# Kernel optimization log

Hardware: AMD Instinct MI355X
Metric: run time of the kernel (lower is better)

The kernel has to match this reference:

```python
import jax, jax.numpy as jnp
import numpy as np

EPS_RHO = 1e-8
EPS_DEN = 1e-9


def _rho_signed_sqrt(x):
    return jnp.sqrt(jax.nn.relu(x) + EPS_RHO) - jnp.sqrt(jax.nn.relu(-x) + EPS_RHO)


def setup_inputs() -> dict:
    key = jax.random.key(0)
    ks = jax.random.split(key, 8)
    B, N, C, A = 2, 512, 1024, 64  # batch, seq, hidden_dim, attn_dim
    s_c = 1.0 / np.sqrt(C)
    s_a = 1.0 / np.sqrt(A)
    return {
        "X": jax.random.normal(ks[0], (B, N, C), jnp.float32),
        "Wq": jax.random.normal(ks[1], (A, C), jnp.float32) * s_c,   # Linear(C->A), no bias
        "Wk": jax.random.normal(ks[2], (A, C), jnp.float32) * s_c,   # Linear(C->A), no bias
        "Wphi": jax.random.normal(ks[3], (A,), jnp.float32) * s_a,   # Linear(A->1), no bias
        "Wy_w": jax.random.normal(ks[4], (C, C), jnp.float32) * s_c, # Linear(C->C)
        "Wy_b": jax.random.normal(ks[5], (C,), jnp.float32) * s_c,
        "We_w": jax.random.normal(ks[6], (C, A), jnp.float32) * s_a, # Linear(A->C)
        "We_b": jax.random.normal(ks[7], (C,), jnp.float32) * s_a,
    }


def reference(X, Wq, Wk, Wphi, Wy_w, Wy_b, We_w, We_b):
    # q, k: (B,N,A); Vy: (B,N,C)
    q = jnp.einsum('bnc,ac->bna', X, Wq)
    k = jnp.einsum('bnc,ac->bna', X, Wk)
    Vy = jnp.einsum('bnc,dc->bnd', X, Wy_w) + Wy_b

    # pairwise features e_ij = relu(rho(q_i + k_j)): (B,N,N,A)
    e = jax.nn.relu(_rho_signed_sqrt(q[:, :, None, :] + k[:, None, :, :]))

    # scores: (B,N,N); stable exp with per-row max (== online-softmax result)
    scores = jnp.einsum('bija,a->bij', e, Wphi)
    m = jnp.max(scores, axis=-1, keepdims=True)
    ex = jnp.exp(scores - m)
    denom = jnp.sum(ex, axis=-1)  # (B,N)

    # part1 = exp_scores @ Vy
    part1 = jnp.einsum('bij,bjc->bic', ex, Vy)
    # part2 = sum_j ex_ij * (We e_ij + be) = We(sum_j ex_ij e_ij) + be * denom  (We is linear)
    Ew = jnp.einsum('bij,bija->bia', ex, e)  # (B,N,A)
    part2 = jnp.einsum('bia,ca->bic', Ew, We_w) + We_b * denom[..., None]

    return (part1 + part2) / (denom[..., None] + EPS_DEN)
```

## Files before the change

kernel.cpp:

```cpp
#include <hip/hip_runtime.h>
#include <math.h>

#define EPS_RHO 1e-8f
#define EPS_DEN 1e-9f

constexpr int Bb = 2;
constexpr int Nn = 512;
constexpr int Cc = 1024;
constexpr int Aa = 64;
constexpr int TOK = Bb * Nn;
constexpr int KG  = 640;

typedef __attribute__((ext_vector_type(8))) short short8;
typedef __attribute__((ext_vector_type(4))) float f32x4;

__device__ __forceinline__ float e_fn(float s) {
    const float SQE = 9.9999994e-05f;
    return sqrtf(fmaxf(s, 0.f) + EPS_RHO) - SQE;
}

__device__ __forceinline__ short f2bf(float x) {
    union { float f; unsigned u; } v; v.f = x;
    unsigned r = v.u + 0x7FFFu + ((v.u >> 16) & 1u);
    return (short)(r >> 16);
}

__device__ __forceinline__ unsigned cvt_pk_bf16(float e0, float e1) {
    unsigned d;
    asm("v_cvt_pk_bf16_f32 %0, %1, %2" : "=v"(d) : "v"(e0), "v"(e1));
    return d;
}

__global__ __launch_bounds__(256) void mega_gemm(
    const float* __restrict__ X,
    const float* __restrict__ Wy_w,
    const float* __restrict__ Wq,
    const float* __restrict__ Wk,
    const float* __restrict__ Wy_b,
    short* __restrict__ Gt,
    float* __restrict__ qg,
    float* __restrict__ kTg)
{
    constexpr int K = 1024, BK = 64;
    __shared__ short As[64][72];
    __shared__ short Bs[64][72];

    int tid = threadIdx.x;
    int bm = blockIdx.y * 64;
    int bn = blockIdx.x * 64;
    int row = tid >> 2;
    int kq  = (tid & 3) << 4;

    const float* ag = X + (size_t)(bm + row) * K + kq;
    int nrow = bn + row;
    const float* bg;
    if (nrow < 1024)      bg = Wy_w + (size_t)nrow * K + kq;
    else if (nrow < 1088) bg = Wq + (size_t)(nrow - 1024) * K + kq;
    else                  bg = Wk + (size_t)(nrow - 1088) * K + kq;

    float4 ar[4], br[4];
    #pragma unroll
    for (int u = 0; u < 4; ++u) {
        ar[u] = *(const float4*)(ag + u * 4);
        br[u] = *(const float4*)(bg + u * 4);
    }

    int wid = tid >> 6, lane = tid & 63;
    int wm = (wid & 1) * 32, wn = (wid >> 1) * 32;
    int fr = lane & 15, fk = (lane >> 4) * 8;

    f32x4 acc[2][2] = {};

    for (int step = 0; step < K / BK; ++step) {
        __syncthreads();
        short tmpA[16], tmpB[16];
        #pragma unroll
        for (int u = 0; u < 4; ++u) {
            tmpA[u*4+0] = f2bf(ar[u].x); tmpA[u*4+1] = f2bf(ar[u].y);
            tmpA[u*4+2] = f2bf(ar[u].z); tmpA[u*4+3] = f2bf(ar[u].w);
            tmpB[u*4+0] = f2bf(br[u].x); tmpB[u*4+1] = f2bf(br[u].y);
            tmpB[u*4+2] = f2bf(br[u].z); tmpB[u*4+3] = f2bf(br[u].w);
        }
        *(short8*)&As[row][kq]     = *(short8*)&tmpA[0];
        *(short8*)&As[row][kq + 8] = *(short8*)&tmpA[8];
        *(short8*)&Bs[row][kq]     = *(short8*)&tmpB[0];
        *(short8*)&Bs[row][kq + 8] = *(short8*)&tmpB[8];
        __syncthreads();

        if (step + 1 < K / BK) {
            const float* ag2 = ag + (size_t)(step + 1) * BK;
            const float* bg2 = bg + (size_t)(step + 1) * BK;
            #pragma unroll
            for (int u = 0; u < 4; ++u) {
                ar[u] = *(const float4*)(ag2 + u * 4);
                br[u] = *(const float4*)(bg2 + u * 4);
            }
        }

        #pragma unroll
        for (int kk = 0; kk < 2; ++kk) {
            short8 af[2], bfr[2];
            #pragma unroll
            for (int mi = 0; mi < 2; ++mi)
                af[mi] = *(const short8*)&As[wm + mi * 16 + fr][kk * 32 + fk];
            #pragma unroll
            for (int ni = 0; ni < 2; ++ni)
                bfr[ni] = *(const short8*)&Bs[wn + ni * 16 + fr][kk * 32 + fk];
            #pragma unroll
            for (int mi = 0; mi < 2; ++mi)
                #pragma unroll
                for (int ni = 0; ni < 2; ++ni)
                    acc[mi][ni] = __builtin_amdgcn_mfma_f32_16x16x32_bf16(
                        af[mi], bfr[ni], acc[mi][ni], 0, 0, 0);
        }
    }

    int cr = (lane >> 4) * 4;
    int cc = lane & 15;
    if (bn < 1024) {
        #pragma unroll
        for (int mi = 0; mi < 2; ++mi)
            #pragma unroll
            for (int ni = 0; ni < 2; ++ni) {
                int c = bn + wn + ni * 16 + cc;
                float bv = Wy_b[c];
                #pragma unroll
                for (int r_ = 0; r_ < 4; ++r_) {
                    int t = bm + wm + mi * 16 + cr + r_;
                    int b = t >> 9, j = t & 511;
                    Gt[((size_t)(b * 1024 + c)) * KG + j] = f2bf(acc[mi][ni][r_] + bv);
                }
            }
    } else if (bn == 1024) {
        #pragma unroll
        for (int mi = 0; mi < 2; ++mi)
            #pragma unroll
            for (int ni = 0; ni < 2; ++ni) {
                int a = wn + ni * 16 + cc;
                #pragma unroll
                for (int r_ = 0; r_ < 4; ++r_) {
                    int t = bm + wm + mi * 16 + cr + r_;
                    qg[(size_t)t * Aa + a] = acc[mi][ni][r_];
                }
            }
    } else {
        #pragma unroll
        for (int mi = 0; mi < 2; ++mi)
            #pragma unroll
            for (int ni = 0; ni < 2; ++ni) {
                int a = wn + ni * 16 + cc;
                #pragma unroll
                for (int r_ = 0; r_ < 4; ++r_) {
                    int t = bm + wm + mi * 16 + cr + r_;
                    int b = t >> 9, j = t & 511;
                    kTg[((size_t)(b * 64 + a)) * 512 + j] = acc[mi][ni][r_];
                }
            }
    }
}

__global__ __launch_bounds__(256) void weprep(
    const float* __restrict__ We_w, short* __restrict__ Gt)
{
    int i = blockIdx.x * 256 + threadIdx.x;
    int s = i & 127;
    int c = (i >> 7) & 1023;
    int b = i >> 17;
    short v = (s < 64) ? f2bf(We_w[(size_t)c * Aa + s]) : (short)0;
    Gt[((size_t)(b * 1024 + c)) * KG + 512 + s] = v;
}

__global__ __launch_bounds__(256) void attn1_fused(
    const float* __restrict__ qg,
    const float* __restrict__ kTg,
    const float* __restrict__ Wphi,
    short* __restrict__ P,
    float* __restrict__ denomg)
{
    __shared__ __align__(16) float qs[Aa];
    __shared__ __align__(16) float wph[Aa];
    __shared__ __align__(16) short E[256][72];
    __shared__ __align__(16) float exs[256];
    __shared__ __align__(16) float red[256];
    __shared__ __align__(16) float ewp[4][Aa];

    int t = blockIdx.x;
    int b = t >> 9;
    int tid = threadIdx.x;

    if (tid < Aa) {
        qs[tid] = qg[(size_t)t * Aa + tid];
        wph[tid] = Wphi[tid];
    }
    __syncthreads();

    const float* kT = kTg + (size_t)b * Aa * 512;

    float dsum = 0.f;
    float ewacc = 0.f;
    int pa = tid & 63;
    int pg = tid >> 6;

    #pragma unroll
    for (int c = 0; c < 2; ++c) {
        int j = c * 256 + tid;

        float s = 0.f;
        #pragma unroll
        for (int a0 = 0; a0 < Aa; a0 += 8) {
            float e[8];
            #pragma unroll
            for (int u = 0; u < 8; ++u) {
                float kv = kT[(size_t)(a0 + u) * 512 + j];
                e[u] = e_fn(qs[a0 + u] + kv);
                s += wph[a0 + u] * e[u];
            }
            uint4 pk;
            pk.x = cvt_pk_bf16(e[0], e[1]);
            pk.y = cvt_pk_bf16(e[2], e[3]);
            pk.z = cvt_pk_bf16(e[4], e[5]);
            pk.w = cvt_pk_bf16(e[6], e[7]);
            *(uint4*)&E[tid][a0] = pk;
        }
        float ex = expf(s);
        exs[tid] = ex;
        dsum += ex;
        P[(size_t)t * KG + j] = f2bf(ex);
        __syncthreads();

        #pragma unroll 8
        for (int jj = 0; jj < 64; ++jj) {
            int jr = pg * 64 + jj;
            unsigned ue = (unsigned)(unsigned short)E[jr][pa];
            float ev = __uint_as_float(ue << 16);
            ewacc += exs[jr] * ev;
        }
        __syncthreads();
    }

    red[tid] = dsum;
    __syncthreads();
    for (int off = 128; off > 0; off >>= 1) {
        if (tid < off) red[tid] += red[tid + off];
        __syncthreads();
    }
    if (tid == 0) denomg[t] = red[0];

    ewp[pg][pa] = ewacc;
    __syncthreads();
    if (tid < Aa) {
        float ew = ewp[0][tid] + ewp[1][tid] + ewp[2][tid] + ewp[3][tid];
        P[(size_t)t * KG + 512 + tid] = f2bf(ew);
    } else if (tid < 128) {
        P[(size_t)t * KG + 576 + (tid - 64)] = 0;
    }
}

__global__ __launch_bounds__(256) void attn2_gemm(
    const short* __restrict__ P,
    const short* __restrict__ Gt,
    const float* __restrict__ We_b,
    const float* __restrict__ denomg,
    float* __restrict__ out)
{
    constexpr int BK = 64, NSTEP = KG / BK;
    __shared__ short As[64][72];
    __shared__ short Bs[64][72];

    int tid = threadIdx.x;
    int bm = blockIdx.y * 64, bn = blockIdx.x * 64;
    int b = bm >> 9;
    int row = tid >> 2;
    int kq  = (tid & 3) << 4;

    const short* ap = P  + (size_t)(bm + row) * KG + kq;
    const short* bp = Gt + ((size_t)(b * 1024 + bn + row)) * KG + kq;

    short8 ar[2], br[2];
    ar[0] = *(const short8*)ap;       ar[1] = *(const short8*)(ap + 8);
    br[0] = *(const short8*)bp;       br[1] = *(const short8*)(bp + 8);

    int wid = tid >> 6, lane = tid & 63;
    int wm = (wid & 1) * 32, wn = (wid >> 1) * 32;
    int fr = lane & 15, fk = (lane >> 4) * 8;

    f32x4 acc[2][2] = {};

    for (int step = 0; step < NSTEP; ++step) {
        __syncthreads();
        *(short8*)&As[row][kq]     = ar[0];
        *(short8*)&As[row][kq + 8] = ar[1];
        *(short8*)&Bs[row][kq]     = br[0];
        *(short8*)&Bs[row][kq + 8] = br[1];
        __syncthreads();

        if (step + 1 < NSTEP) {
            const short* ap2 = ap + (size_t)(step + 1) * BK;
            const short* bp2 = bp + (size_t)(step + 1) * BK;
            ar[0] = *(const short8*)ap2;  ar[1] = *(const short8*)(ap2 + 8);
            br[0] = *(const short8*)bp2;  br[1] = *(const short8*)(bp2 + 8);
        }

        #pragma unroll
        for (int kk = 0; kk < 2; ++kk) {
            short8 af[2], bfr[2];
            #pragma unroll
            for (int mi = 0; mi < 2; ++mi)
                af[mi] = *(const short8*)&As[wm + mi * 16 + fr][kk * 32 + fk];
            #pragma unroll
            for (int ni = 0; ni < 2; ++ni)
                bfr[ni] = *(const short8*)&Bs[wn + ni * 16 + fr][kk * 32 + fk];
            #pragma unroll
            for (int mi = 0; mi < 2; ++mi)
                #pragma unroll
                for (int ni = 0; ni < 2; ++ni)
                    acc[mi][ni] = __builtin_amdgcn_mfma_f32_16x16x32_bf16(
                        af[mi], bfr[ni], acc[mi][ni], 0, 0, 0);
        }
    }

    int cr = (lane >> 4) * 4;
    int cc = lane & 15;
    #pragma unroll
    for (int mi = 0; mi < 2; ++mi)
        #pragma unroll
        for (int ni = 0; ni < 2; ++ni) {
            int c = bn + wn + ni * 16 + cc;
            float bv = We_b[c];
            #pragma unroll
            for (int r_ = 0; r_ < 4; ++r_) {
                int t = bm + wm + mi * 16 + cr + r_;
                float dn = denomg[t];
                out[(size_t)t * Cc + c] = (acc[mi][ni][r_] + bv * dn) / (dn + EPS_DEN);
            }
        }
}

extern "C" void kernel_launch(void* const* d_in, const int* in_sizes, int n_in,
                              void* d_out, int out_size, void* d_ws, size_t ws_size,
                              hipStream_t stream)
{
    const float* X    = (const float*)d_in[0];
    const float* Wq   = (const float*)d_in[1];
    const float* Wk   = (const float*)d_in[2];
    const float* Wphi = (const float*)d_in[3];
    const float* Wy_w = (const float*)d_in[4];
    const float* Wy_b = (const float*)d_in[5];
    const float* We_w = (const float*)d_in[6];
    const float* We_b = (const float*)d_in[7];
    float* out = (float*)d_out;

    float* ws = (float*)d_ws;
    float* qg     = ws;
    float* kTg    = qg + (size_t)TOK * Aa;
    float* denomg = kTg + (size_t)TOK * Aa;
    short* Gt     = (short*)(denomg + 1024);
    short* P      = Gt + (size_t)2 * 1024 * KG;

    weprep<<<1024, 256, 0, stream>>>(We_w, Gt);

    dim3 gg(18, 16);
    mega_gemm<<<gg, 256, 0, stream>>>(X, Wy_w, Wq, Wk, Wy_b, Gt, qg, kTg);

    attn1_fused<<<TOK, 256, 0, stream>>>(qg, kTg, Wphi, P, denomg);

    dim3 g2(16, 16);
    attn2_gemm<<<g2, 256, 0, stream>>>(P, Gt, We_b, denomg, out);
}
```

Measured before the change: 122.8 us.

## Pre-convert GEMM inputs to bf16, shrink K padding, widen Ew reduction

Adds a prep kernel that converts X, Wy_w, Wq, Wk and We_w to bf16 once, so mega_gemm loads half the bytes and skips the per-tile f2bf conversion. The padded K dimension of the second GEMM drops from 640 to 576, removing one zero K-step and the zero-fill writes. The Ew accumulation in attn1 now reads two bf16 values per lane across 8 groups. The cost is an extra full read and write pass over X and the weights in the prep kernel.

```diff
diff --git a/kernel.cpp b/kernel.cpp
--- a/kernel.cpp
+++ b/kernel.cpp
@@ -9,9 +9,10 @@
 constexpr int Cc = 1024;
 constexpr int Aa = 64;
 constexpr int TOK = Bb * Nn;
-constexpr int KG  = 640;
+constexpr int KGP = 576;
 
 typedef __attribute__((ext_vector_type(8))) short short8;
+typedef __attribute__((ext_vector_type(4))) short short4v;
 typedef __attribute__((ext_vector_type(4))) float f32x4;
 
 __device__ __forceinline__ float e_fn(float s) {
@@ -31,11 +32,47 @@
     return d;
 }
 
+constexpr int PREP_N0 = 1024 * 1024;
+constexpr int PREP_N1 = 1152 * 1024;
+constexpr int PREP_N2 = 2 * 1024 * 64;
+constexpr int PREP_TOT = PREP_N0 + PREP_N1 + PREP_N2;
+
+__global__ __launch_bounds__(256) void prep_kernel(
+    const float* __restrict__ X, const float* __restrict__ Wy_w,
+    const float* __restrict__ Wq, const float* __restrict__ Wk,
+    const float* __restrict__ We_w,
+    short* __restrict__ Xb, short* __restrict__ Wb, short* __restrict__ Gt)
+{
+    int g = (blockIdx.x * 256 + threadIdx.x) * 4;
+    if (g >= PREP_TOT) return;
+
+    const float* src;
+    short* dst;
+    if (g < PREP_N0) {
+        src = X + g;
+        dst = Xb + g;
+    } else if (g < PREP_N0 + PREP_N1) {
+        int i2 = g - PREP_N0;
+        if (i2 < 1048576)       src = Wy_w + i2;
+        else if (i2 < 1114112)  src = Wq + (i2 - 1048576);
+        else                    src = Wk + (i2 - 1114112);
+        dst = Wb + i2;
+    } else {
+        int i3 = g - PREP_N0 - PREP_N1;
+        int b = i3 >> 16;
+        int r = i3 & 65535;
+        int c = r >> 6, a = r & 63;
+        src = We_w + (size_t)c * Aa + a;
+        dst = Gt + ((size_t)(b * 1024 + c)) * KGP + 512 + a;
+    }
+    float4 v = *(const float4*)src;
+    short4v o = { f2bf(v.x), f2bf(v.y), f2bf(v.z), f2bf(v.w) };
+    *(short4v*)dst = o;
+}
+
 __global__ __launch_bounds__(256) void mega_gemm(
-    const float* __restrict__ X,
-    const float* __restrict__ Wy_w,
-    const float* __restrict__ Wq,
-    const float* __restrict__ Wk,
+    const short* __restrict__ Xb,
+    const short* __restrict__ Wb,
     const float* __restrict__ Wy_b,
     short* __restrict__ Gt,
     float* __restrict__ qg,
@@ -51,19 +88,12 @@
     int row = tid >> 2;
     int kq  = (tid & 3) << 4;
 
-    const float* ag = X + (size_t)(bm + row) * K + kq;
-    int nrow = bn + row;
-    const float* bg;
-    if (nrow < 1024)      bg = Wy_w + (size_t)nrow * K + kq;
-    else if (nrow < 1088) bg = Wq + (size_t)(nrow - 1024) * K + kq;
-    else                  bg = Wk + (size_t)(nrow - 1088) * K + kq;
-
-    float4 ar[4], br[4];
-    #pragma unroll
-    for (int u = 0; u < 4; ++u) {
-        ar[u] = *(const float4*)(ag + u * 4);
-        br[u] = *(const float4*)(bg + u * 4);
-    }
+    const short* ag = Xb + (size_t)(bm + row) * K + kq;
+    const short* bg = Wb + (size_t)(bn + row) * K + kq;
+
+    short8 ar[2], br[2];
+    ar[0] = *(const short8*)ag;       ar[1] = *(const short8*)(ag + 8);
+    br[0] = *(const short8*)bg;       br[1] = *(const short8*)(bg + 8);
 
     int wid = tid >> 6, lane = tid & 63;
     int wm = (wid & 1) * 32, wn = (wid >> 1) * 32;
@@ -73,28 +103,17 @@
 
     for (int step = 0; step < K / BK; ++step) {
         __syncthreads();
-        short tmpA[16], tmpB[16];
-        #pragma unroll
-        for (int u = 0; u < 4; ++u) {
-            tmpA[u*4+0] = f2bf(ar[u].x); tmpA[u*4+1] = f2bf(ar[u].y);
-            tmpA[u*4+2] = f2bf(ar[u].z); tmpA[u*4+3] = f2bf(ar[u].w);
-            tmpB[u*4+0] = f2bf(br[u].x); tmpB[u*4+1] = f2bf(br[u].y);
-            tmpB[u*4+2] = f2bf(br[u].z); tmpB[u*4+3] = f2bf(br[u].w);
-        }
-        *(short8*)&As[row][kq]     = *(short8*)&tmpA[0];
-        *(short8*)&As[row][kq + 8] = *(short8*)&tmpA[8];
-        *(short8*)&Bs[row][kq]     = *(short8*)&tmpB[0];
-        *(short8*)&Bs[row][kq + 8] = *(short8*)&tmpB[8];
+        *(short8*)&As[row][kq]     = ar[0];
+        *(short8*)&As[row][kq + 8] = ar[1];
+        *(short8*)&Bs[row][kq]     = br[0];
+        *(short8*)&Bs[row][kq + 8] = br[1];
         __syncthreads();
 
         if (step + 1 < K / BK) {
-            const float* ag2 = ag + (size_t)(step + 1) * BK;
-            const float* bg2 = bg + (size_t)(step + 1) * BK;
-            #pragma unroll
-            for (int u = 0; u < 4; ++u) {
-                ar[u] = *(const float4*)(ag2 + u * 4);
-                br[u] = *(const float4*)(bg2 + u * 4);
-            }
+            const short* ag2 = ag + (size_t)(step + 1) * BK;
+            const short* bg2 = bg + (size_t)(step + 1) * BK;
+            ar[0] = *(const short8*)ag2;  ar[1] = *(const short8*)(ag2 + 8);
+            br[0] = *(const short8*)bg2;  br[1] = *(const short8*)(bg2 + 8);
         }
 
         #pragma unroll
@@ -128,7 +147,7 @@
                 for (int r_ = 0; r_ < 4; ++r_) {
                     int t = bm + wm + mi * 16 + cr + r_;
                     int b = t >> 9, j = t & 511;
-                    Gt[((size_t)(b * 1024 + c)) * KG + j] = f2bf(acc[mi][ni][r_] + bv);
+                    Gt[((size_t)(b * 1024 + c)) * KGP + j] = f2bf(acc[mi][ni][r_] + bv);
                 }
             }
     } else if (bn == 1024) {
@@ -157,17 +176,6 @@
                 }
             }
     }
-}
-
-__global__ __launch_bounds__(256) void weprep(
-    const float* __restrict__ We_w, short* __restrict__ Gt)
-{
-    int i = blockIdx.x * 256 + threadIdx.x;
-    int s = i & 127;
-    int c = (i >> 7) & 1023;
-    int b = i >> 17;
-    short v = (s < 64) ? f2bf(We_w[(size_t)c * Aa + s]) : (short)0;
-    Gt[((size_t)(b * 1024 + c)) * KG + 512 + s] = v;
 }
 
 __global__ __launch_bounds__(256) void attn1_fused(
@@ -182,7 +190,7 @@
     __shared__ __align__(16) short E[256][72];
     __shared__ __align__(16) float exs[256];
     __shared__ __align__(16) float red[256];
-    __shared__ __align__(16) float ewp[4][Aa];
+    __shared__ __align__(16) float ewp[8][Aa];
 
     int t = blockIdx.x;
     int b = t >> 9;
@@ -197,9 +205,9 @@
     const float* kT = kTg + (size_t)b * Aa * 512;
 
     float dsum = 0.f;
-    float ewacc = 0.f;
-    int pa = tid & 63;
-    int pg = tid >> 6;
+    float ew0 = 0.f, ew1 = 0.f;
+    int pa2 = (tid & 31) * 2;
+    int pg8 = tid >> 5;
 
     #pragma unroll
     for (int c = 0; c < 2; ++c) {
@@ -225,15 +233,18 @@
         float ex = expf(s);
         exs[tid] = ex;
         dsum += ex;
-        P[(size_t)t * KG + j] = f2bf(ex);
+        P[(size_t)t * KGP + j] = f2bf(ex);
         __syncthreads();
 
         #pragma unroll 8
-        for (int jj = 0; jj < 64; ++jj) {
-            int jr = pg * 64 + jj;
-            unsigned ue = (unsigned)(unsigned short)E[jr][pa];
-            float ev = __uint_as_float(ue << 16);
-            ewacc += exs[jr] * ev;
+        for (int jj = 0; jj < 32; ++jj) {
+            int jr = pg8 * 32 + jj;
+            unsigned ue = *(const unsigned*)&E[jr][pa2];
+            float e0 = __uint_as_float(ue << 16);
+            float e1 = __uint_as_float(ue & 0xFFFF0000u);
+            float x = exs[jr];
+            ew0 += x * e0;
+            ew1 += x * e1;
         }
         __syncthreads();
     }
@@ -246,13 +257,14 @@
     }
     if (tid == 0) denomg[t] = red[0];
 
-    ewp[pg][pa] = ewacc;
+    ewp[pg8][pa2] = ew0;
+    ewp[pg8][pa2 + 1] = ew1;
     __syncthreads();
     if (tid < Aa) {
-        float ew = ewp[0][tid] + ewp[1][tid] + ewp[2][tid] + ewp[3][tid];
-        P[(size_t)t * KG + 512 + tid] = f2bf(ew);
-    } else if (tid < 128) {
-        P[(size_t)t * KG + 576 + (tid - 64)] = 0;
+        float ew = 0.f;
+        #pragma unroll
+        for (int g = 0; g < 8; ++g) ew += ewp[g][tid];
+        P[(size_t)t * KGP + 512 + tid] = f2bf(ew);
     }
 }
 
@@ -263,7 +275,7 @@
     const float* __restrict__ denomg,
     float* __restrict__ out)
 {
-    constexpr int BK = 64, NSTEP = KG / BK;
+    constexpr int BK = 64, NSTEP = KGP / BK;
     __shared__ short As[64][72];
     __shared__ short Bs[64][72];
 
@@ -273,8 +285,8 @@
     int row = tid >> 2;
     int kq  = (tid & 3) << 4;
 
-    const short* ap = P  + (size_t)(bm + row) * KG + kq;
-    const short* bp = Gt + ((size_t)(b * 1024 + bn + row)) * KG + kq;
+    const short* ap = P  + (size_t)(bm + row) * KGP + kq;
+    const short* bp = Gt + ((size_t)(b * 1024 + bn + row)) * KGP + kq;
 
     short8 ar[2], br[2];
     ar[0] = *(const short8*)ap;       ar[1] = *(const short8*)(ap + 8);
@@ -354,13 +366,16 @@
     float* qg     = ws;
     float* kTg    = qg + (size_t)TOK * Aa;
     float* denomg = kTg + (size_t)TOK * Aa;
-    short* Gt     = (short*)(denomg + 1024);
-    short* P      = Gt + (size_t)2 * 1024 * KG;
-
-    weprep<<<1024, 256, 0, stream>>>(We_w, Gt);
+    short* Xb     = (short*)(denomg + 1024);
+    short* Wb     = Xb + (size_t)1024 * 1024;
+    short* Gt     = Wb + (size_t)1152 * 1024;
+    short* P      = Gt + (size_t)2 * 1024 * KGP;
+
+    prep_kernel<<<(PREP_TOT / 4 + 255) / 256, 256, 0, stream>>>(
+        X, Wy_w, Wq, Wk, We_w, Xb, Wb, Gt);
 
     dim3 gg(18, 16);
-    mega_gemm<<<gg, 256, 0, stream>>>(X, Wy_w, Wq, Wk, Wy_b, Gt, qg, kTg);
+    mega_gemm<<<gg, 256, 0, stream>>>(Xb, Wb, Wy_b, Gt, qg, kTg);
 
     attn1_fused<<<TOK, 256, 0, stream>>>(qg, kTg, Wphi, P, denomg);
 
```

New measurement: 121.8 us. No clear change (-0.8%).
